# Kernel optimization log

Measured on AMD Instinct MI355X. Metric: run time of the kernel, lower is better.

The kernel has to match this reference:

```python
import jax, jax.numpy as jnp
import numpy as np

N_EMBD = 1024
N_HEAD = 16
HEAD_SIZE = 64
LN_EPS = 1e-3  # keras LayerNormalization default


def setup_inputs() -> dict:
    key = jax.random.key(0)
    ks = jax.random.split(key, 7)
    B, S, D, H, E = 4, 2048, N_EMBD, N_HEAD, HEAD_SIZE
    x = jax.random.normal(ks[0], (B, S, D), dtype=jnp.float32)
    scale = 1.0 / np.sqrt(D)
    Wq = jax.random.normal(ks[1], (H, D, E), dtype=jnp.float32) * scale
    Wk = jax.random.normal(ks[2], (H, D, E), dtype=jnp.float32) * scale
    Wv = jax.random.normal(ks[3], (H, D, E), dtype=jnp.float32) * scale
    Wo = jax.random.normal(ks[4], (H * E, D), dtype=jnp.float32) * scale
    gamma = jnp.ones((D,), dtype=jnp.float32)
    beta = jnp.zeros((D,), dtype=jnp.float32)
    return {"x": x, "Wq": Wq, "Wk": Wk, "Wv": Wv, "Wo": Wo,
            "gamma": gamma, "beta": beta}


def reference(x, Wq, Wk, Wv, Wo, gamma, beta):
    B, S, D = x.shape
    H, _, E = Wq.shape
    q = jnp.einsum('bsd,hde->bhse', x, Wq)
    k = jnp.einsum('bsd,hde->bhse', x, Wk)
    v = jnp.einsum('bsd,hde->bhse', x, Wv)
    scores = jnp.einsum('bhse,bhte->bhst', q, k)  # [B,H,S,S]
    causal = jnp.tril(jnp.ones((S, S), dtype=bool))
    # original: mask with -inf, then divide by sqrt(head_size) -> same result
    scores = jnp.where(causal, scores / jnp.sqrt(jnp.float32(E)),
                       jnp.float32(-jnp.inf))
    attn = jax.nn.softmax(scores, axis=-1)
    out = jnp.einsum('bhst,bhte->bhse', attn, v)
    heads = out.transpose(0, 2, 1, 3).reshape(B, S, H * E)  # concat heads
    y = x + heads @ Wo
    # keras LayerNormalization (axis=-1, eps=1e-3)
    mu = jnp.mean(y, axis=-1, keepdims=True)
    var = jnp.mean(jnp.square(y - mu), axis=-1, keepdims=True)
    y = (y - mu) * jax.lax.rsqrt(var + LN_EPS) * gamma + beta
    return y
```

## Files before the change

### kernel.cpp

```cpp
#include <hip/hip_runtime.h>
#include <stdint.h>

typedef __bf16 bf16;
typedef float  f32x4  __attribute__((ext_vector_type(4)));
typedef float  float4v __attribute__((ext_vector_type(4)));
typedef bf16   bf16x8 __attribute__((ext_vector_type(8)));
typedef bf16   bf16x4 __attribute__((ext_vector_type(4)));

#define B_ 4
#define S_ 2048
#define D_ 1024
#define H_ 16
#define E_ 64
#define M_ 8192
#define QSCALE 0.18033688f


__device__ __forceinline__ void async_ld16(const bf16* g, bf16* l) {
  __builtin_amdgcn_global_load_lds(
      (const __attribute__((address_space(1))) void*)g,
      (__attribute__((address_space(3))) void*)l, 16, 0, 0);
}


__global__ __launch_bounds__(256) void pack_x(const float* __restrict__ x,
                                              bf16* __restrict__ xb, int n4) {
  int i = blockIdx.x * 256 + threadIdx.x;
  if (i < n4) {
    float4v v = ((const float4v*)x)[i];
    bf16x4 o = { (bf16)v.x, (bf16)v.y, (bf16)v.z, (bf16)v.w };
    ((bf16x4*)xb)[i] = o;
  }
}

__global__ __launch_bounds__(256) void pack_wqkv(const float* __restrict__ Wq,
                                                 const float* __restrict__ Wk,
                                                 const float* __restrict__ Wv,
                                                 bf16* __restrict__ Bt) {
  __shared__ float t[64][65];
  const int mat = blockIdx.x;
  const int qkv = mat >> 4, h = mat & 15;
  const float* W = (qkv == 0) ? Wq : ((qkv == 1) ? Wk : Wv);
  const float* src = W + h * (D_ * E_);
  const int d0 = blockIdx.y * 64;
  const int tr = threadIdx.x >> 2;
  const int tc = (threadIdx.x & 3) * 16;
  for (int i = 0; i < 16; ++i) t[tr][tc + i] = src[(d0 + tr) * E_ + tc + i];
  __syncthreads();
  const int n = qkv * 1024 + h * 64 + tr;
  bf16* dst = Bt + n * D_ + d0 + tc;
  for (int i = 0; i < 16; ++i) dst[i] = (bf16)t[tc + i][tr];
}

__global__ __launch_bounds__(256) void pack_wo(const float* __restrict__ Wo,
                                               bf16* __restrict__ Wot) {
  __shared__ float t[64][65];
  const int k0 = blockIdx.x * 64, n0 = blockIdx.y * 64;
  const int tr = threadIdx.x >> 2;
  const int tc = (threadIdx.x & 3) * 16;
  for (int i = 0; i < 16; ++i) t[tr][tc + i] = Wo[(k0 + tr) * D_ + n0 + tc + i];
  __syncthreads();
  bf16* dst = Wot + (n0 + tr) * D_ + k0 + tc;
  for (int i = 0; i < 16; ++i) dst[i] = (bf16)t[tc + i][tr];
}


template <int EPI>
__global__ __launch_bounds__(256, 2) void gemm128(
    const bf16* __restrict__ A, const bf16* __restrict__ Bt, int K,
    bf16* __restrict__ qo, bf16* __restrict__ ko, bf16* __restrict__ vt,
    const float* __restrict__ xres, float* __restrict__ outp) {
  __shared__ bf16 As[128 * 64];
  __shared__ bf16 Bs[128 * 64];
  const int tid = threadIdx.x;
  const int wave = tid >> 6, lane = tid & 63;
  const int lm = lane & 15, quad = lane >> 4;
  const int wr = wave >> 1, wc = wave & 1;
  const int m0 = blockIdx.y * 128, n0 = blockIdx.x * 128;
  f32x4 acc[4][4] = {};

  for (int kt = 0; kt < K; kt += 64) {
    for (int it = 0; it < 4; ++it) {
      int cl = it * 256 + tid;
      int r = cl >> 3, pc = cl & 7;
      int cc = pc ^ (r & 7);
      async_ld16(A + (m0 + r) * K + kt + cc * 8, As + cl * 8);
      async_ld16(Bt + (n0 + r) * K + kt + cc * 8, Bs + cl * 8);
    }
    __syncthreads();
    for (int kk = 0; kk < 64; kk += 32) {
      bf16x8 af[4], bfr[4];
      const int ccb = (kk >> 3) + quad;
      for (int i = 0; i < 4; ++i) {
        int row = wr * 64 + i * 16 + lm;
        af[i] = *(const bf16x8*)(As + row * 64 + (ccb ^ (row & 7)) * 8);
      }
      for (int j = 0; j < 4; ++j) {
        int row = wc * 64 + j * 16 + lm;
        bfr[j] = *(const bf16x8*)(Bs + row * 64 + (ccb ^ (row & 7)) * 8);
      }
      for (int i = 0; i < 4; ++i)
        for (int j = 0; j < 4; ++j)
          acc[i][j] = __builtin_amdgcn_mfma_f32_16x16x32_bf16(af[i], bfr[j], acc[i][j], 0, 0, 0);
    }
    __syncthreads();
  }

  if (EPI == 0) {
    const int qkv = n0 >> 10;
    const int hh = ((n0 + wc * 64) >> 6) & 15;
    for (int i = 0; i < 4; ++i) {
      const int gm0 = m0 + wr * 64 + i * 16 + quad * 4;
      const int b = gm0 >> 11, s0 = gm0 & 2047;
      for (int j = 0; j < 4; ++j) {
        const int e = j * 16 + lm;
        if (qkv == 2) {
          bf16x4 pv = { (bf16)acc[i][j][0], (bf16)acc[i][j][1],
                        (bf16)acc[i][j][2], (bf16)acc[i][j][3] };
          *(bf16x4*)(vt + (((b << 4) + hh) * 64 + e) * (size_t)S_ + s0) = pv;
        } else if (qkv == 0) {
          for (int r = 0; r < 4; ++r)
            qo[(((b << 4) + hh) * S_ + (s0 + r)) * (size_t)E_ + e] =
                (bf16)(acc[i][j][r] * QSCALE);
        } else {
          for (int r = 0; r < 4; ++r)
            ko[(((b << 4) + hh) * S_ + (s0 + r)) * (size_t)E_ + e] = (bf16)acc[i][j][r];
        }
      }
    }
  } else {
    for (int i = 0; i < 4; ++i)
      for (int r = 0; r < 4; ++r) {
        const int gm = m0 + wr * 64 + i * 16 + quad * 4 + r;
        for (int j = 0; j < 4; ++j) {
          const int gn = n0 + wc * 64 + j * 16 + lm;
          outp[gm * (size_t)D_ + gn] = acc[i][j][r] + xres[gm * (size_t)D_ + gn];
        }
      }
  }
}


__global__ __launch_bounds__(256, 4) void attn(
    const bf16* __restrict__ Q, const bf16* __restrict__ Kb,
    const bf16* __restrict__ Vt, bf16* __restrict__ Hd) {
  __shared__ __align__(16) bf16 Ks[2][64 * 64];
  __shared__ __align__(16) bf16 Vs[2][64 * 64];
  __shared__ __align__(16) bf16 Pb[4][16 * 64];
  const int tid = threadIdx.x;
  const int w = tid >> 6, lane = tid & 63;
  const int lm = lane & 15, quad = lane >> 4;
  const int l7 = lm & 7;
  const int bi = blockIdx.x;
  const int bh = bi & 63;
  const int qA = bi >> 6;
  const int qB = 31 - qA;
  const bf16* Qp = Q + (size_t)bh * S_ * E_;
  const bf16* Kp = Kb + (size_t)bh * S_ * E_;
  const bf16* Vp = Vt + (size_t)bh * E_ * S_;

  int qb[2], sq[2];
  bf16x8 qf[2][2];
  qb[0] = qA * 64 + w * 16;
  qb[1] = qB * 64 + w * 16;
#pragma unroll
  for (int t = 0; t < 2; ++t) {
    sq[t] = qb[t] + lm;
    qf[t][0] = *(const bf16x8*)(Qp + sq[t] * E_ + quad * 8);
    qf[t][1] = *(const bf16x8*)(Qp + sq[t] * E_ + 32 + quad * 8);
  }
  float ls[2] = { 0.0f, 0.0f };
  f32x4 oacc[2][4] = {};

  for (int j = 0; j <= qB; ++j) {
    const int p = j & 1;
    const int sk0 = j * 64;
#pragma unroll
    for (int it = 0; it < 2; ++it) {
      int cl = it * 256 + tid;
      int r = cl >> 3, pc = cl & 7;
      int cc = pc ^ (r & 7);
      async_ld16(Kp + (sk0 + r) * E_ + cc * 8, &Ks[p][cl * 8]);
      async_ld16(Vp + (size_t)r * S_ + sk0 + cc * 8, &Vs[p][cl * 8]);
    }
    __syncthreads();

#pragma unroll
    for (int t = 0; t < 2; ++t) {
      const int d = (qb[t] - sk0) >> 4;
      if (d < 0) continue;
      f32x4 st[4] = {};
#pragma unroll
      for (int i = 0; i < 4; ++i) {
        const int row = i * 16 + lm;
        bf16x8 k0 = *(const bf16x8*)(&Ks[p][row * 64 + (quad ^ l7) * 8]);
        st[i] = __builtin_amdgcn_mfma_f32_16x16x32_bf16(k0, qf[t][0], st[i], 0, 0, 0);
        bf16x8 k1 = *(const bf16x8*)(&Ks[p][row * 64 + ((4 + quad) ^ l7) * 8]);
        st[i] = __builtin_amdgcn_mfma_f32_16x16x32_bf16(k1, qf[t][1], st[i], 0, 0, 0);
      }
      if (d < 4) {
#pragma unroll
        for (int i = 0; i < 4; ++i) {
          const int base = (i - d) * 16 + quad * 4;
#pragma unroll
          for (int r = 0; r < 4; ++r)
            st[i][r] = (base + r > lm) ? -30000.0f : st[i][r];
        }
      }
      char* pbase = (char*)&Pb[w][0];
#pragma unroll
      for (int i = 0; i < 4; ++i) {
        const float p0 = __builtin_amdgcn_exp2f(st[i][0]);
        const float p1 = __builtin_amdgcn_exp2f(st[i][1]);
        const float p2 = __builtin_amdgcn_exp2f(st[i][2]);
        const float p3 = __builtin_amdgcn_exp2f(st[i][3]);
        ls[t] += (p0 + p1) + (p2 + p3);
        bf16x4 pv = { (bf16)p0, (bf16)p1, (bf16)p2, (bf16)p3 };
        const int c = (i * 2 + (quad >> 1)) ^ l7;
        *(bf16x4*)(pbase + lm * 128 + c * 16 + (quad & 1) * 8) = pv;
      }
#pragma unroll
      for (int ks = 0; ks < 2; ++ks) {
        bf16x8 pf = *(const bf16x8*)(pbase + lm * 128 + ((ks * 4 + quad) ^ l7) * 16);
#pragma unroll
        for (int te = 0; te < 4; ++te) {
          const int vrow = te * 16 + lm;
          bf16x8 vf = *(const bf16x8*)(&Vs[p][vrow * 64 + ((ks * 4 + quad) ^ l7) * 8]);
          oacc[t][te] = __builtin_amdgcn_mfma_f32_16x16x32_bf16(vf, pf, oacc[t][te], 0, 0, 0);
        }
      }
    }
  }
  const int b = bh >> 4, h = bh & 15;
#pragma unroll
  for (int t = 0; t < 2; ++t) {
    float rs = ls[t];
    rs += __shfl_xor(rs, 16);
    rs += __shfl_xor(rs, 32);
    const float inv = 1.0f / rs;
#pragma unroll
    for (int te = 0; te < 4; ++te) {
      bf16x4 ov = { (bf16)(oacc[t][te][0] * inv), (bf16)(oacc[t][te][1] * inv),
                    (bf16)(oacc[t][te][2] * inv), (bf16)(oacc[t][te][3] * inv) };
      *(bf16x4*)(&Hd[((size_t)b * S_ + sq[t]) * D_ + h * 64 + te * 16 + quad * 4]) = ov;
    }
  }
}


__global__ __launch_bounds__(256) void lnorm(float* __restrict__ y,
                                             const float* __restrict__ gamma,
                                             const float* __restrict__ beta) {
  const int row = blockIdx.x, tid = threadIdx.x;
  float4v v = ((const float4v*)y)[row * 256 + tid];
  float s = v.x + v.y + v.z + v.w;
  float ss = v.x * v.x + v.y * v.y + v.z * v.z + v.w * v.w;
#pragma unroll
  for (int o = 1; o < 64; o <<= 1) { s += __shfl_xor(s, o); ss += __shfl_xor(ss, o); }
  __shared__ float sb[8];
  const int wv = tid >> 6, lane = tid & 63;
  if (lane == 0) { sb[wv] = s; sb[4 + wv] = ss; }
  __syncthreads();
  s = sb[0] + sb[1] + sb[2] + sb[3];
  ss = sb[4] + sb[5] + sb[6] + sb[7];
  const float mu = s * (1.0f / 1024.0f);
  const float var = ss * (1.0f / 1024.0f) - mu * mu;
  const float rstd = rsqrtf(var + 1e-3f);
  float4v g = ((const float4v*)gamma)[tid];
  float4v bb = ((const float4v*)beta)[tid];
  float4v o;
  o.x = (v.x - mu) * rstd * g.x + bb.x;
  o.y = (v.y - mu) * rstd * g.y + bb.y;
  o.z = (v.z - mu) * rstd * g.z + bb.z;
  o.w = (v.w - mu) * rstd * g.w + bb.w;
  ((float4v*)y)[row * 256 + tid] = o;
}


extern "C" void kernel_launch(void* const* d_in, const int* in_sizes, int n_in,
                              void* d_out, int out_size, void* d_ws, size_t ws_size,
                              hipStream_t stream) {
  const float* x     = (const float*)d_in[0];
  const float* Wq    = (const float*)d_in[1];
  const float* Wk    = (const float*)d_in[2];
  const float* Wv    = (const float*)d_in[3];
  const float* Wo    = (const float*)d_in[4];
  const float* gamma = (const float*)d_in[5];
  const float* beta  = (const float*)d_in[6];
  float* out = (float*)d_out;

  char* ws = (char*)d_ws;
  bf16* xb    = (bf16*)(ws);
  bf16* wqkvt = (bf16*)(ws + 16777216);
  bf16* wot   = (bf16*)(ws + 23068672);
  bf16* Qb    = (bf16*)(ws + 25165824);
  bf16* Kb    = (bf16*)(ws + 41943040);
  bf16* Vtb   = (bf16*)(ws + 58720256);
  bf16* heads = xb;

  pack_x<<<M_ * D_ / 4 / 256, 256, 0, stream>>>(x, xb, M_ * D_ / 4);
  pack_wqkv<<<dim3(48, 16), 256, 0, stream>>>(Wq, Wk, Wv, wqkvt);
  pack_wo<<<dim3(16, 16), 256, 0, stream>>>(Wo, wot);
  gemm128<0><<<dim3(24, 64), 256, 0, stream>>>(xb, wqkvt, D_, Qb, Kb, Vtb, nullptr, nullptr);
  attn<<<64 * 16, 256, 0, stream>>>(Qb, Kb, Vtb, heads);
  gemm128<1><<<dim3(8, 64), 256, 0, stream>>>(heads, wot, D_, nullptr, nullptr, nullptr, x, out);
  lnorm<<<M_, 256, 0, stream>>>(out, gamma, beta);
}
```

Measured before the change: 252.5 us.

## Keep softmax probabilities in registers via fp16 16x16x16 MFMA for PV

Stores V in fp16 and converts the exponentiated scores to packed fp16 in registers. These feed 16x16x16 f16 MFMAs directly, which removes the per-wave LDS round-trip for P and its shared buffer. It also interleaves the QK^T MFMAs of both query tiles so each K fragment load is shared, and simplifies the diagonal masking check. The cost is twice as many PV MFMA instructions (k=16 instead of 32) and fp16 range/precision for V and P in place of bf16.

```diff
diff --git a/kernel.cpp b/kernel.cpp
--- a/kernel.cpp
+++ b/kernel.cpp
@@ -2,10 +2,12 @@
 #include <stdint.h>
 
 typedef __bf16 bf16;
-typedef float  f32x4  __attribute__((ext_vector_type(4)));
-typedef float  float4v __attribute__((ext_vector_type(4)));
-typedef bf16   bf16x8 __attribute__((ext_vector_type(8)));
-typedef bf16   bf16x4 __attribute__((ext_vector_type(4)));
+typedef float   f32x4   __attribute__((ext_vector_type(4)));
+typedef float   float4v __attribute__((ext_vector_type(4)));
+typedef bf16    bf16x8  __attribute__((ext_vector_type(8)));
+typedef bf16    bf16x4  __attribute__((ext_vector_type(4)));
+typedef __fp16  half2   __attribute__((ext_vector_type(2)));
+typedef __fp16  half4   __attribute__((ext_vector_type(4)));
 
 #define B_ 4
 #define S_ 2048
@@ -16,7 +18,7 @@
 #define QSCALE 0.18033688f
 
 
-__device__ __forceinline__ void async_ld16(const bf16* g, bf16* l) {
+__device__ __forceinline__ void async_ld16(const void* g, void* l) {
   __builtin_amdgcn_global_load_lds(
       (const __attribute__((address_space(1))) void*)g,
       (__attribute__((address_space(3))) void*)l, 16, 0, 0);
@@ -115,9 +117,9 @@
       for (int j = 0; j < 4; ++j) {
         const int e = j * 16 + lm;
         if (qkv == 2) {
-          bf16x4 pv = { (bf16)acc[i][j][0], (bf16)acc[i][j][1],
-                        (bf16)acc[i][j][2], (bf16)acc[i][j][3] };
-          *(bf16x4*)(vt + (((b << 4) + hh) * 64 + e) * (size_t)S_ + s0) = pv;
+          half4 pv = { (__fp16)acc[i][j][0], (__fp16)acc[i][j][1],
+                       (__fp16)acc[i][j][2], (__fp16)acc[i][j][3] };
+          *(half4*)(vt + (((b << 4) + hh) * 64 + e) * (size_t)S_ + s0) = pv;
         } else if (qkv == 0) {
           for (int r = 0; r < 4; ++r)
             qo[(((b << 4) + hh) * S_ + (s0 + r)) * (size_t)E_ + e] =
@@ -146,11 +148,11 @@
     const bf16* __restrict__ Vt, bf16* __restrict__ Hd) {
   __shared__ __align__(16) bf16 Ks[2][64 * 64];
   __shared__ __align__(16) bf16 Vs[2][64 * 64];
-  __shared__ __align__(16) bf16 Pb[4][16 * 64];
   const int tid = threadIdx.x;
   const int w = tid >> 6, lane = tid & 63;
   const int lm = lane & 15, quad = lane >> 4;
   const int l7 = lm & 7;
+  const int qh = quad >> 1, qb1 = quad & 1;
   const int bi = blockIdx.x;
   const int bh = bi & 63;
   const int qA = bi >> 6;
@@ -185,52 +187,63 @@
     }
     __syncthreads();
 
+    const bool act0 = (j <= qA);
+
+    f32x4 st[2][4] = {};
+#pragma unroll
+    for (int i = 0; i < 4; ++i) {
+      const int row = i * 16 + lm;
+      bf16x8 k0 = *(const bf16x8*)(&Ks[p][row * 64 + (quad ^ l7) * 8]);
+      bf16x8 k1 = *(const bf16x8*)(&Ks[p][row * 64 + ((4 + quad) ^ l7) * 8]);
+      st[1][i] = __builtin_amdgcn_mfma_f32_16x16x32_bf16(k0, qf[1][0], st[1][i], 0, 0, 0);
+      st[1][i] = __builtin_amdgcn_mfma_f32_16x16x32_bf16(k1, qf[1][1], st[1][i], 0, 0, 0);
+      if (act0) {
+        st[0][i] = __builtin_amdgcn_mfma_f32_16x16x32_bf16(k0, qf[0][0], st[0][i], 0, 0, 0);
+        st[0][i] = __builtin_amdgcn_mfma_f32_16x16x32_bf16(k1, qf[0][1], st[0][i], 0, 0, 0);
+      }
+    }
+
+    half4 pb[2][4];
 #pragma unroll
     for (int t = 0; t < 2; ++t) {
-      const int d = (qb[t] - sk0) >> 4;
-      if (d < 0) continue;
-      f32x4 st[4] = {};
+      if (t == 0 && !act0) continue;
+      const bool diag = (t == 0) ? (j == qA) : (j == qB);
+      if (diag) {
+#pragma unroll
+        for (int i = 0; i < 4; ++i) {
+          const int base = (i - w) * 16 + quad * 4;
+#pragma unroll
+          for (int r = 0; r < 4; ++r)
+            st[t][i][r] = (base + r > lm) ? -30000.0f : st[t][i][r];
+        }
+      }
 #pragma unroll
       for (int i = 0; i < 4; ++i) {
-        const int row = i * 16 + lm;
-        bf16x8 k0 = *(const bf16x8*)(&Ks[p][row * 64 + (quad ^ l7) * 8]);
-        st[i] = __builtin_amdgcn_mfma_f32_16x16x32_bf16(k0, qf[t][0], st[i], 0, 0, 0);
-        bf16x8 k1 = *(const bf16x8*)(&Ks[p][row * 64 + ((4 + quad) ^ l7) * 8]);
-        st[i] = __builtin_amdgcn_mfma_f32_16x16x32_bf16(k1, qf[t][1], st[i], 0, 0, 0);
-      }
-      if (d < 4) {
-#pragma unroll
-        for (int i = 0; i < 4; ++i) {
-          const int base = (i - d) * 16 + quad * 4;
-#pragma unroll
-          for (int r = 0; r < 4; ++r)
-            st[i][r] = (base + r > lm) ? -30000.0f : st[i][r];
-        }
-      }
-      char* pbase = (char*)&Pb[w][0];
+        const float p0 = __builtin_amdgcn_exp2f(st[t][i][0]);
+        const float p1 = __builtin_amdgcn_exp2f(st[t][i][1]);
+        const float p2 = __builtin_amdgcn_exp2f(st[t][i][2]);
+        const float p3 = __builtin_amdgcn_exp2f(st[t][i][3]);
+        ls[t] += (p0 + p1) + (p2 + p3);
+        half2 lo = __builtin_amdgcn_cvt_pkrtz(p0, p1);
+        half2 hi = __builtin_amdgcn_cvt_pkrtz(p2, p3);
+        pb[t][i] = __builtin_shufflevector(lo, hi, 0, 1, 2, 3);
+      }
+    }
+
+#pragma unroll
+    for (int te = 0; te < 4; ++te) {
+      const int row = te * 16 + lm;
 #pragma unroll
       for (int i = 0; i < 4; ++i) {
-        const float p0 = __builtin_amdgcn_exp2f(st[i][0]);
-        const float p1 = __builtin_amdgcn_exp2f(st[i][1]);
-        const float p2 = __builtin_amdgcn_exp2f(st[i][2]);
-        const float p3 = __builtin_amdgcn_exp2f(st[i][3]);
-        ls[t] += (p0 + p1) + (p2 + p3);
-        bf16x4 pv = { (bf16)p0, (bf16)p1, (bf16)p2, (bf16)p3 };
-        const int c = (i * 2 + (quad >> 1)) ^ l7;
-        *(bf16x4*)(pbase + lm * 128 + c * 16 + (quad & 1) * 8) = pv;
-      }
-#pragma unroll
-      for (int ks = 0; ks < 2; ++ks) {
-        bf16x8 pf = *(const bf16x8*)(pbase + lm * 128 + ((ks * 4 + quad) ^ l7) * 16);
-#pragma unroll
-        for (int te = 0; te < 4; ++te) {
-          const int vrow = te * 16 + lm;
-          bf16x8 vf = *(const bf16x8*)(&Vs[p][vrow * 64 + ((ks * 4 + quad) ^ l7) * 8]);
-          oacc[t][te] = __builtin_amdgcn_mfma_f32_16x16x32_bf16(vf, pf, oacc[t][te], 0, 0, 0);
-        }
-      }
-    }
-  }
+        const int c = (2 * i + qh) ^ l7;
+        half4 vf = *(const half4*)(&Vs[p][row * 64 + c * 8 + qb1 * 4]);
+        oacc[1][te] = __builtin_amdgcn_mfma_f32_16x16x16f16(vf, pb[1][i], oacc[1][te], 0, 0, 0);
+        if (act0)
+          oacc[0][te] = __builtin_amdgcn_mfma_f32_16x16x16f16(vf, pb[0][i], oacc[0][te], 0, 0, 0);
+      }
+    }
+  }
+
   const int b = bh >> 4, h = bh & 15;
 #pragma unroll
   for (int t = 0; t < 2; ++t) {
```

Result: slower. 259.5 us (+2.8%).
